# Kernel tuning notes

Measured on AMD Instinct MI355X. Metric: run time of the kernel, lower is better.

Reference implementation:

```python
import jax, jax.numpy as jnp
import numpy as np

N_NODES = 170000
N_EDGES = 1200000
IN_FEATS = 128
N_HIDDEN = 256
N_CLASSES = 40
BN_EPS = 1e-5


def setup_inputs() -> dict:
    key = jax.random.key(0)
    ks = jax.random.split(key, 12)
    feat = jax.random.normal(ks[0], (N_NODES, IN_FEATS), dtype=jnp.float32)
    src = jax.random.randint(ks[1], (N_EDGES,), 0, N_NODES, dtype=jnp.int32)
    dst = jax.random.randint(ks[2], (N_EDGES,), 0, N_NODES, dtype=jnp.int32)
    # GraphConv weights (glorot-ish scale) and last-layer bias
    W0 = jax.random.normal(ks[3], (IN_FEATS, N_HIDDEN), dtype=jnp.float32) * (1.0 / np.sqrt(IN_FEATS))
    W1 = jax.random.normal(ks[4], (N_HIDDEN, N_HIDDEN), dtype=jnp.float32) * (1.0 / np.sqrt(N_HIDDEN))
    W2 = jax.random.normal(ks[5], (N_HIDDEN, N_CLASSES), dtype=jnp.float32) * (1.0 / np.sqrt(N_HIDDEN))
    b2 = jnp.zeros((N_CLASSES,), dtype=jnp.float32)
    # BatchNorm affine params for the two hidden layers
    g0 = jnp.ones((N_HIDDEN,), dtype=jnp.float32)
    beta0 = jnp.zeros((N_HIDDEN,), dtype=jnp.float32)
    g1 = jnp.ones((N_HIDDEN,), dtype=jnp.float32)
    beta1 = jnp.zeros((N_HIDDEN,), dtype=jnp.float32)
    return {"feat": feat, "src": src, "dst": dst, "W0": W0, "W1": W1, "W2": W2,
            "b2": b2, "g0": g0, "beta0": beta0, "g1": g1, "beta1": beta1}


def _batchnorm(h, gamma, beta):
    mean = jnp.mean(h, axis=0)
    var = jnp.mean((h - mean) ** 2, axis=0)  # biased var, torch training-mode norm
    return (h - mean) * jax.lax.rsqrt(var + BN_EPS) * gamma + beta


def reference(feat, src, dst, W0, W1, W2, b2, g0, beta0, g1, beta1):
    n = feat.shape[0]
    ones_e = jnp.ones(src.shape, dtype=feat.dtype)
    deg_out = jnp.clip(jax.ops.segment_sum(ones_e, src, num_segments=n), 1.0)
    deg_in = jnp.clip(jax.ops.segment_sum(ones_e, dst, num_segments=n), 1.0)
    norm_src = deg_out ** -0.5  # [N]
    norm_dst = deg_in ** -0.5   # [N]

    def conv(h, W, bias=None):
        # GraphConv 'both': D_out^{-1/2} message, sum-aggregate, D_in^{-1/2}
        h = h @ W                              # project first (out <= in)
        msg = h[src] * norm_src[src][:, None]  # [E, out]
        agg = jax.ops.segment_sum(msg, dst, num_segments=n) * norm_dst[:, None]
        if bias is not None:
            agg = agg + bias
        return agg

    # dropout layers are identity in this deterministic (eval-style) reference
    h = conv(feat, W0)
    h = jax.nn.relu(_batchnorm(h, g0, beta0))
    h = conv(h, W1)
    h = jax.nn.relu(_batchnorm(h, g1, beta1))
    h = conv(h, W2, b2)
    return h
```

## Files before the change

### kernel.cpp

```cpp
#include <hip/hip_runtime.h>

#define NN 170000
#define NE 1200000
#define F_IN 128
#define F_HID 256
#define F_OUT 40
#define BN_EPS 1e-5f
#define SCAN_B ((NN + 255) / 256)
#define GB32 ((NN + 31) / 32)
#define GB128 ((NN + 127) / 128)
#define STAT_ROWS GB32
#define STAT_CHUNK 32
#define STAT_NCH ((STAT_ROWS + STAT_CHUNK - 1) / STAT_CHUNK)

typedef __attribute__((ext_vector_type(8))) short short8;
typedef __attribute__((ext_vector_type(4))) float f32x4;
typedef __attribute__((ext_vector_type(4))) unsigned short us4;
typedef __attribute__((ext_vector_type(4))) unsigned int u32x4;

__device__ __forceinline__ float b2f(unsigned short u) {
    union { unsigned x; float f; } c; c.x = ((unsigned)u) << 16; return c.f;
}
__device__ __forceinline__ unsigned short f2b(float f) {
    union { float f; unsigned x; } c; c.f = f;
    unsigned r = (c.x + 0x7FFFu + ((c.x >> 16) & 1u)) >> 16;
    return (unsigned short)r;
}
__device__ __forceinline__ unsigned bn2(unsigned u, float a0, float b0, float a1, float b1) {
    float lo = b2f((unsigned short)(u & 0xffffu));
    float hi = b2f((unsigned short)(u >> 16));
    lo = fmaxf(lo * a0 + b0, 0.0f);
    hi = fmaxf(hi * a1 + b1, 0.0f);
    return (unsigned)f2b(lo) | ((unsigned)f2b(hi) << 16);
}

__device__ __forceinline__ void agg_sum(const u32x4& v, float (&aa)[8]) {
    aa[0] += b2f((unsigned short)(v.x & 0xffffu)); aa[1] += b2f((unsigned short)(v.x >> 16));
    aa[2] += b2f((unsigned short)(v.y & 0xffffu)); aa[3] += b2f((unsigned short)(v.y >> 16));
    aa[4] += b2f((unsigned short)(v.z & 0xffffu)); aa[5] += b2f((unsigned short)(v.z >> 16));
    aa[6] += b2f((unsigned short)(v.w & 0xffffu)); aa[7] += b2f((unsigned short)(v.w >> 16));
}
__device__ __forceinline__ void agg_fuse(const u32x4& v, float ns,
        const f32x4& ca0, const f32x4& ca1, const f32x4& cb0, const f32x4& cb1, float (&aa)[8]) {
    aa[0] += fmaxf(fmaf(b2f((unsigned short)(v.x & 0xffffu)), ca0.x, cb0.x), 0.f) * ns;
    aa[1] += fmaxf(fmaf(b2f((unsigned short)(v.x >> 16)),     ca0.y, cb0.y), 0.f) * ns;
    aa[2] += fmaxf(fmaf(b2f((unsigned short)(v.y & 0xffffu)), ca0.z, cb0.z), 0.f) * ns;
    aa[3] += fmaxf(fmaf(b2f((unsigned short)(v.y >> 16)),     ca0.w, cb0.w), 0.f) * ns;
    aa[4] += fmaxf(fmaf(b2f((unsigned short)(v.z & 0xffffu)), ca1.x, cb1.x), 0.f) * ns;
    aa[5] += fmaxf(fmaf(b2f((unsigned short)(v.z >> 16)),     ca1.y, cb1.y), 0.f) * ns;
    aa[6] += fmaxf(fmaf(b2f((unsigned short)(v.w & 0xffffu)), ca1.z, cb1.z), 0.f) * ns;
    aa[7] += fmaxf(fmaf(b2f((unsigned short)(v.w >> 16)),     ca1.w, cb1.w), 0.f) * ns;
}

__global__ void count_kernel(const int* __restrict__ src, const int* __restrict__ dst,
                             int* __restrict__ cnt_src, int* __restrict__ cnt_dst, int E) {
    int e = blockIdx.x * blockDim.x + threadIdx.x;
    if (e < E) {
        atomicAdd(&cnt_src[src[e]], 1);
        atomicAdd(&cnt_dst[dst[e]], 1);
    }
}

__global__ void norm_kernel(const int* __restrict__ cnt_src, const int* __restrict__ cnt_dst,
                            float* __restrict__ norm_src, float* __restrict__ norm_dst, int N) {
    int i = blockIdx.x * blockDim.x + threadIdx.x;
    if (i < N) {
        norm_src[i] = rsqrtf((float)max(cnt_src[i], 1));
        norm_dst[i] = rsqrtf((float)max(cnt_dst[i], 1));
    }
}

__global__ void scan_block_kernel(const int* __restrict__ cnt, int* __restrict__ local,
                                  int* __restrict__ partials, int N) {
    __shared__ int s[256];
    int t = threadIdx.x;
    int idx = blockIdx.x * 256 + t;
    int v = (idx < N) ? cnt[idx] : 0;
    s[t] = v;
    __syncthreads();
    #pragma unroll
    for (int off = 1; off < 256; off <<= 1) {
        int x = (t >= off) ? s[t - off] : 0;
        __syncthreads();
        s[t] += x;
        __syncthreads();
    }
    if (idx < N) local[idx] = s[t] - v;
    if (t == 255) partials[blockIdx.x] = s[t];
}

__global__ void scan_partials_kernel(int* __restrict__ partials, int B) {
    __shared__ int s[1024];
    int t = threadIdx.x;
    int v = (t < B) ? partials[t] : 0;
    s[t] = v;
    __syncthreads();
    #pragma unroll
    for (int off = 1; off < 1024; off <<= 1) {
        int x = (t >= off) ? s[t - off] : 0;
        __syncthreads();
        s[t] += x;
        __syncthreads();
    }
    if (t < B) partials[t] = s[t] - v;
}

__global__ void scan_add_kernel(const int* __restrict__ local, const int* __restrict__ partials,
                                int* __restrict__ row_ptr, int N) {
    int idx = blockIdx.x * blockDim.x + threadIdx.x;
    if (idx < N) row_ptr[idx] = local[idx] + partials[idx >> 8];
    if (idx == 0) row_ptr[N] = NE;
}

__global__ void fill_kernel(const int* __restrict__ src, const int* __restrict__ dst,
                            const int* __restrict__ row_ptr, int* __restrict__ fill,
                            int* __restrict__ csr_src, int E) {
    int e = blockIdx.x * blockDim.x + threadIdx.x;
    if (e < E) {
        int d = dst[e];
        int pos = row_ptr[d] + atomicAdd(&fill[d], 1);
        csr_src[pos] = src[e];
    }
}

__global__ void cast_feat_kernel(const float* __restrict__ feat, const float* __restrict__ norm_src,
                                 unsigned short* __restrict__ featb) {
    unsigned idx = blockIdx.x * blockDim.x + threadIdx.x;
    if (idx >= (unsigned)NN * (F_IN / 4)) return;
    float ns = norm_src[idx / (F_IN / 4)];
    f32x4 v = __builtin_nontemporal_load((const f32x4*)(feat + (size_t)idx * 4));
    us4 o; o.x = f2b(v.x * ns); o.y = f2b(v.y * ns); o.z = f2b(v.z * ns); o.w = f2b(v.w * ns);
    *(us4*)(featb + (size_t)idx * 4) = o;
}

template<int K, int M, int MP>
__global__ void wt_kernel(const float* __restrict__ W, unsigned short* __restrict__ Wt) {
    int idx = blockIdx.x * blockDim.x + threadIdx.x;
    if (idx >= MP * K) return;
    int m = idx / K, k = idx % K;
    float v = (m < M) ? W[(size_t)k * M + m] : 0.0f;
    Wt[idx] = f2b(v);
}

__global__ void stat_reduce_kernel(const float* __restrict__ part, float* __restrict__ red) {
    int c = threadIdx.x;
    int ch = blockIdx.x;
    int r0 = ch * STAT_CHUNK;
    int r1 = min(r0 + STAT_CHUNK, STAT_ROWS);
    float s = 0.f;
    for (int r = r0; r < r1; r++) s += part[(size_t)r * 512 + c];
    red[ch * 512 + c] = s;
}

__global__ void bn_finalize2_kernel(const float* __restrict__ red,
                                    const float* __restrict__ gamma, const float* __restrict__ beta,
                                    float* __restrict__ a, float* __restrict__ b) {
    int c = threadIdx.x;
    float sum = 0.f, sumsq = 0.f;
    for (int ch = 0; ch < STAT_NCH; ch++) {
        sum   += red[ch * 512 + c];
        sumsq += red[ch * 512 + 256 + c];
    }
    float invN = 1.0f / (float)NN;
    float mean = sum * invN;
    float var = sumsq * invN - mean * mean;
    float inv = rsqrtf(var + BN_EPS);
    float ac = inv * gamma[c];
    a[c] = ac;
    b[c] = beta[c] - mean * ac;
}

template<int F, int WM_T, int WN_T, int WAVES_N, bool FUSE>
__global__ __launch_bounds__(256) void fused_gather_gemm(
        const unsigned short* __restrict__ h,
        const int* __restrict__ row_ptr, const int* __restrict__ csr_src,
        const float* __restrict__ bna, const float* __restrict__ bnb,
        const unsigned short* __restrict__ Wt,
        const float* __restrict__ norm_src, const float* __restrict__ norm_dst,
        void* __restrict__ C, float* __restrict__ opart, int N) {
    constexpr int WAVES_M = 4 / WAVES_N;
    constexpr int BM = WM_T * 16 * WAVES_M;
    constexpr int LPN = F / 8;
    constexpr int NPW = 64 / LPN;
    constexpr int NPB = BM / 4;
    __shared__ unsigned short As[BM * F];

    const int lane = threadIdx.x & 63;
    const int wave = threadIdx.x >> 6;
    const int r0 = blockIdx.x * BM;

    {
        const int sub = lane / LPN;
        const int cl = lane % LPN;
        f32x4 ca0 = {0,0,0,0}, ca1 = {0,0,0,0}, cb0 = {0,0,0,0}, cb1 = {0,0,0,0};
        if (FUSE) {
            ca0 = *(const f32x4*)(bna + cl * 8);
            ca1 = *(const f32x4*)(bna + cl * 8 + 4);
            cb0 = *(const f32x4*)(bnb + cl * 8);
            cb1 = *(const f32x4*)(bnb + cl * 8 + 4);
        }
        #pragma unroll
        for (int g = 0; g < NPB / NPW; g++) {
            int nl = wave * NPB + g * NPW + sub;
            int node = r0 + nl;
            float aa[8] = {0.f, 0.f, 0.f, 0.f, 0.f, 0.f, 0.f, 0.f};
            int beg = 0, end = 0;
            if (node < N) { beg = row_ptr[node]; end = row_ptr[node + 1]; }
            int e = beg;
            for (; e + 2 <= end; e += 2) {
                int s0 = csr_src[e], s1 = csr_src[e + 1];
                u32x4 v0 = *(const u32x4*)(h + (size_t)s0 * F + cl * 8);
                u32x4 v1 = *(const u32x4*)(h + (size_t)s1 * F + cl * 8);
                if (FUSE) {
                    float n0 = norm_src[s0], n1 = norm_src[s1];
                    agg_fuse(v0, n0, ca0, ca1, cb0, cb1, aa);
                    agg_fuse(v1, n1, ca0, ca1, cb0, cb1, aa);
                } else {
                    agg_sum(v0, aa); agg_sum(v1, aa);
                }
            }
            if (e < end) {
                int s0 = csr_src[e];
                u32x4 v0 = *(const u32x4*)(h + (size_t)s0 * F + cl * 8);
                if (FUSE) agg_fuse(v0, norm_src[s0], ca0, ca1, cb0, cb1, aa);
                else      agg_sum(v0, aa);
            }
            u32x4 d;
            d.x = (unsigned)f2b(aa[0]) | ((unsigned)f2b(aa[1]) << 16);
            d.y = (unsigned)f2b(aa[2]) | ((unsigned)f2b(aa[3]) << 16);
            d.z = (unsigned)f2b(aa[4]) | ((unsigned)f2b(aa[5]) << 16);
            d.w = (unsigned)f2b(aa[6]) | ((unsigned)f2b(aa[7]) << 16);
            unsigned off = ((unsigned)(nl * (F * 2) + cl * 16)) ^ (((unsigned)nl & 7u) << 4);
            *(u32x4*)((char*)As + off) = d;
        }
    }
    __syncthreads();

    const int quad = lane >> 4, l15 = lane & 15;
    const int wr = wave / WAVES_N, wc = wave % WAVES_N;
    const int wmb = wr * WM_T * 16;
    const int wnb = wc * WN_T * 16;

    const unsigned short* bptr[WN_T];
    #pragma unroll
    for (int j = 0; j < WN_T; j++)
        bptr[j] = Wt + (size_t)(wnb + j * 16 + l15) * F + quad * 8;

    f32x4 acc[WM_T][WN_T] = {};
    #pragma unroll
    for (int kk = 0; kk < F; kk += 32) {
        short8 af[WM_T], bf[WN_T];
        #pragma unroll
        for (int i = 0; i < WM_T; i++) {
            int row = wmb + i * 16 + l15;
            unsigned off = ((unsigned)(row * (F * 2) + (kk + quad * 8) * 2)) ^ (((unsigned)row & 7u) << 4);
            af[i] = *(const short8*)((const char*)As + off);
        }
        #pragma unroll
        for (int j = 0; j < WN_T; j++)
            bf[j] = *(const short8*)(bptr[j] + kk);
        #pragma unroll
        for (int i = 0; i < WM_T; i++)
            #pragma unroll
            for (int j = 0; j < WN_T; j++)
                acc[i][j] = __builtin_amdgcn_mfma_f32_16x16x32_bf16(af[i], bf[j], acc[i][j], 0, 0, 0);
    }

    float s[WN_T] = {}, ss[WN_T] = {};
    #pragma unroll
    for (int i = 0; i < WM_T; i++) {
        #pragma unroll
        for (int r = 0; r < 4; r++) {
            int row = r0 + wmb + i * 16 + quad * 4 + r;
            if (row >= N) continue;
            float nd = norm_dst[row];
            #pragma unroll
            for (int j = 0; j < WN_T; j++) {
                float v = acc[i][j][r] * nd;
                int col = wnb + j * 16 + l15;
                s[j] += v; ss[j] += v * v;
                ((unsigned short*)C)[(size_t)row * F_HID + col] = f2b(v);
            }
        }
    }
    #pragma unroll
    for (int j = 0; j < WN_T; j++) {
        float t = s[j], t2 = ss[j];
        t  += __shfl_xor(t, 16);  t  += __shfl_xor(t, 32);
        t2 += __shfl_xor(t2, 16); t2 += __shfl_xor(t2, 32);
        if (quad == 0) {
            int col = wnb + j * 16 + l15;
            size_t prow = (size_t)(blockIdx.x * WAVES_M + wr) * 512;
            opart[prow + col] = t;
            opart[prow + 256 + col] = t2;
        }
    }
}

__global__ __launch_bounds__(256, 3) void gemm2_kernel(const unsigned short* __restrict__ A,
                                                       const unsigned short* __restrict__ Wt,
                                                       const float* __restrict__ norm_src,
                                                       const float* __restrict__ bna,
                                                       const float* __restrict__ bnb,
                                                       float* __restrict__ C, int N) {
    constexpr int K = 256, WM_T = 2, WN_T = 4;
    const int lane = threadIdx.x & 63;
    const int wave = threadIdx.x >> 6;
    const int quad = lane >> 4, l15 = lane & 15;
    const int r0 = blockIdx.x * 128;
    const int wmb = wave * WM_T * 16;

    const unsigned short* aptr[WM_T];
    #pragma unroll
    for (int i = 0; i < WM_T; i++) {
        int gr = r0 + wmb + i * 16 + l15;
        if (gr > N - 1) gr = N - 1;
        aptr[i] = A + (size_t)gr * K + quad * 8;
    }
    const unsigned short* bptr[WN_T];
    #pragma unroll
    for (int j = 0; j < WN_T; j++)
        bptr[j] = Wt + (size_t)(j * 16 + l15) * K + quad * 8;

    f32x4 acc[WM_T][WN_T] = {};
    #pragma unroll
    for (int kk = 0; kk < K; kk += 32) {
        int kb = kk + quad * 8;
        const f32x4 a0 = *(const f32x4*)(bna + kb);
        const f32x4 a1 = *(const f32x4*)(bna + kb + 4);
        const f32x4 s0 = *(const f32x4*)(bnb + kb);
        const f32x4 s1 = *(const f32x4*)(bnb + kb + 4);
        short8 af[WM_T], bf[WN_T];
        #pragma unroll
        for (int i = 0; i < WM_T; i++) {
            u32x4 u = *(const u32x4*)(aptr[i] + kk);
            u.x = bn2(u.x, a0.x, s0.x, a0.y, s0.y);
            u.y = bn2(u.y, a0.z, s0.z, a0.w, s0.w);
            u.z = bn2(u.z, a1.x, s1.x, a1.y, s1.y);
            u.w = bn2(u.w, a1.z, s1.z, a1.w, s1.w);
            af[i] = *(short8*)&u;
        }
        #pragma unroll
        for (int j = 0; j < WN_T; j++)
            bf[j] = *(const short8*)(bptr[j] + kk);
        #pragma unroll
        for (int i = 0; i < WM_T; i++)
            #pragma unroll
            for (int j = 0; j < WN_T; j++)
                acc[i][j] = __builtin_amdgcn_mfma_f32_16x16x32_bf16(af[i], bf[j], acc[i][j], 0, 0, 0);
    }

    #pragma unroll
    for (int i = 0; i < WM_T; i++) {
        #pragma unroll
        for (int r = 0; r < 4; r++) {
            int row = r0 + wmb + i * 16 + quad * 4 + r;
            if (row >= N) continue;
            float ns = norm_src[row];
            #pragma unroll
            for (int j = 0; j < WN_T; j++) {
                int col = j * 16 + l15;
                if (col < F_OUT)
                    C[(size_t)row * F_OUT + col] = acc[i][j][r] * ns;
            }
        }
    }
}

__global__ void gather_final_kernel(const float* __restrict__ h, const int* __restrict__ row_ptr,
                                    const int* __restrict__ csr_src,
                                    const float* __restrict__ norm_dst, const float* __restrict__ bias,
                                    float* __restrict__ out, int N) {
    constexpr int TPN = F_OUT / 4;
    unsigned idx = blockIdx.x * blockDim.x + threadIdx.x;
    if (idx >= (unsigned)N * TPN) return;
    unsigned node = idx / TPN;
    unsigned g = idx % TPN;
    int beg = row_ptr[node], end = row_ptr[node + 1];
    float ax0 = 0.f, ay0 = 0.f, az0 = 0.f, aw0 = 0.f;
    float ax1 = 0.f, ay1 = 0.f, az1 = 0.f, aw1 = 0.f;
    int e = beg;
    for (; e + 2 <= end; e += 2) {
        int s0 = csr_src[e], s1 = csr_src[e + 1];
        const f32x4 v0 = *(const f32x4*)(h + (size_t)s0 * F_OUT + g * 4);
        const f32x4 v1 = *(const f32x4*)(h + (size_t)s1 * F_OUT + g * 4);
        ax0 += v0.x; ay0 += v0.y; az0 += v0.z; aw0 += v0.w;
        ax1 += v1.x; ay1 += v1.y; az1 += v1.z; aw1 += v1.w;
    }
    if (e < end) {
        int s0 = csr_src[e];
        const f32x4 v0 = *(const f32x4*)(h + (size_t)s0 * F_OUT + g * 4);
        ax0 += v0.x; ay0 += v0.y; az0 += v0.z; aw0 += v0.w;
    }
    float nd = norm_dst[node];
    const f32x4 b = *(const f32x4*)(bias + g * 4);
    f32x4 r;
    r.x = (ax0 + ax1) * nd + b.x; r.y = (ay0 + ay1) * nd + b.y;
    r.z = (az0 + az1) * nd + b.z; r.w = (aw0 + aw1) * nd + b.w;
    __builtin_nontemporal_store(r, (f32x4*)(out + (size_t)node * F_OUT + g * 4));
}

extern "C" void kernel_launch(void* const* d_in, const int* in_sizes, int n_in,
                              void* d_out, int out_size, void* d_ws, size_t ws_size,
                              hipStream_t stream) {
    const float* feat  = (const float*)d_in[0];
    const int*   src   = (const int*)d_in[1];
    const int*   dst   = (const int*)d_in[2];
    const float* W0    = (const float*)d_in[3];
    const float* W1    = (const float*)d_in[4];
    const float* W2    = (const float*)d_in[5];
    const float* b2    = (const float*)d_in[6];
    const float* g0    = (const float*)d_in[7];
    const float* beta0 = (const float*)d_in[8];
    const float* g1    = (const float*)d_in[9];
    const float* beta1 = (const float*)d_in[10];
    float* out = (float*)d_out;

    const int N = NN, E = NE;

    char* ws = (char*)d_ws;
    auto alloc_b = [&](size_t bytes) {
        void* p = (void*)ws;
        ws += ((bytes + 255) / 256) * 256;
        return p;
    };
    float* norm_src = (float*)alloc_b((size_t)N * 4);
    float* norm_dst = (float*)alloc_b((size_t)N * 4);
    int*   row_ptr  = (int*)alloc_b((size_t)(N + 1) * 4);
    int*   csr_src  = (int*)alloc_b((size_t)E * 4);
    float* bnpart   = (float*)alloc_b((size_t)STAT_ROWS * 512 * 4);
    float* bnred    = (float*)alloc_b((size_t)STAT_NCH * 512 * 4);
    float* bn_a0    = (float*)alloc_b(256 * 4);
    float* bn_b0    = (float*)alloc_b(256 * 4);
    float* bn_a1    = (float*)alloc_b(256 * 4);
    float* bn_b1    = (float*)alloc_b(256 * 4);
    unsigned short* Wt0 = (unsigned short*)alloc_b((size_t)256 * 128 * 2);
    unsigned short* Wt1 = (unsigned short*)alloc_b((size_t)256 * 256 * 2);
    unsigned short* Wt2 = (unsigned short*)alloc_b((size_t)64 * 256 * 2);
    void* B1 = alloc_b((size_t)N * 512);
    void* B2 = alloc_b((size_t)N * 512);
    unsigned short* featb = (unsigned short*)alloc_b((size_t)N * F_IN * 2);

    unsigned short* B1b = (unsigned short*)B1;
    unsigned short* B2b = (unsigned short*)B2;
    float*          B1f = (float*)B1;

    int* cnt_src  = (int*)B1;
    int* cnt_dst  = cnt_src + N;
    int* fill     = cnt_dst + N;
    int* local    = fill + N;
    int* partials = local + N;

    hipMemsetAsync(cnt_src, 0, ((size_t)4 * N + 1024) * 4, stream);
    count_kernel<<<(E + 255) / 256, 256, 0, stream>>>(src, dst, cnt_src, cnt_dst, E);
    norm_kernel<<<(N + 255) / 256, 256, 0, stream>>>(cnt_src, cnt_dst, norm_src, norm_dst, N);
    scan_block_kernel<<<SCAN_B, 256, 0, stream>>>(cnt_dst, local, partials, N);
    scan_partials_kernel<<<1, 1024, 0, stream>>>(partials, SCAN_B);
    scan_add_kernel<<<(N + 255) / 256, 256, 0, stream>>>(local, partials, row_ptr, N);
    fill_kernel<<<(E + 255) / 256, 256, 0, stream>>>(src, dst, row_ptr, fill, csr_src, E);
    wt_kernel<128, 256, 256><<<(256 * 128 + 255) / 256, 256, 0, stream>>>(W0, Wt0);
    wt_kernel<256, 256, 256><<<(256 * 256 + 255) / 256, 256, 0, stream>>>(W1, Wt1);
    wt_kernel<256, 40, 64><<<(64 * 256 + 255) / 256, 256, 0, stream>>>(W2, Wt2);
    cast_feat_kernel<<<((unsigned)N * (F_IN / 4) + 255) / 256, 256, 0, stream>>>(feat, norm_src, featb);

    fused_gather_gemm<128, 2, 4, 4, false><<<GB32, 256, 0, stream>>>(
        featb, row_ptr, csr_src, nullptr, nullptr, Wt0, nullptr, norm_dst, B1, bnpart, N);
    stat_reduce_kernel<<<STAT_NCH, 512, 0, stream>>>(bnpart, bnred);
    bn_finalize2_kernel<<<1, 256, 0, stream>>>(bnred, g0, beta0, bn_a0, bn_b0);

    fused_gather_gemm<256, 2, 4, 4, true><<<GB32, 256, 0, stream>>>(
        B1b, row_ptr, csr_src, bn_a0, bn_b0, Wt1, norm_src, norm_dst, B2, bnpart, N);
    stat_reduce_kernel<<<STAT_NCH, 512, 0, stream>>>(bnpart, bnred);
    bn_finalize2_kernel<<<1, 256, 0, stream>>>(bnred, g1, beta1, bn_a1, bn_b1);

    gemm2_kernel<<<GB128, 256, 0, stream>>>(B2b, Wt2, norm_src, bn_a1, bn_b1, B1f, N);
    {
        unsigned total = (unsigned)N * (F_OUT / 4);
        gather_final_kernel<<<(total + 255) / 256, 256, 0, stream>>>(
            B1f, row_ptr, csr_src, norm_dst, b2, out, N);
    }
}
```

Measured before the change: 763.6 us.

## Make each wave own 16 rows independently in fused gather-GEMM, drop block barrier

Each wave now gathers its own 16 destination rows into a private LDS slice and computes all 256 output columns for them, looping over 16 column tiles. This removes the block-wide __syncthreads between gather and GEMM, so waves with short neighbour lists can move on without waiting for the slowest wave. Blocks now cover 64 rows instead of 32, with matching changes to the BN partial-stat row count. The cost is less reuse of weight fragments: every wave streams the whole W matrix from global or L2 memory per 16 rows, and each MFMA chain now works on a single accumulator, which gives less instruction-level parallelism.

```diff
diff --git a/kernel.cpp b/kernel.cpp
--- a/kernel.cpp
+++ b/kernel.cpp
@@ -7,9 +7,9 @@
 #define F_OUT 40
 #define BN_EPS 1e-5f
 #define SCAN_B ((NN + 255) / 256)
-#define GB32 ((NN + 31) / 32)
+#define GB64 ((NN + 63) / 64)
 #define GB128 ((NN + 127) / 128)
-#define STAT_ROWS GB32
+#define STAT_ROWS (4 * GB64)
 #define STAT_CHUNK 32
 #define STAT_NCH ((STAT_ROWS + STAT_CHUNK - 1) / STAT_CHUNK)
 
@@ -170,7 +170,7 @@
     b[c] = beta[c] - mean * ac;
 }
 
-template<int F, int WM_T, int WN_T, int WAVES_N, bool FUSE>
+template<int F, bool FUSE>
 __global__ __launch_bounds__(256) void fused_gather_gemm(
         const unsigned short* __restrict__ h,
         const int* __restrict__ row_ptr, const int* __restrict__ csr_src,
@@ -178,16 +178,15 @@
         const unsigned short* __restrict__ Wt,
         const float* __restrict__ norm_src, const float* __restrict__ norm_dst,
         void* __restrict__ C, float* __restrict__ opart, int N) {
-    constexpr int WAVES_M = 4 / WAVES_N;
-    constexpr int BM = WM_T * 16 * WAVES_M;
     constexpr int LPN = F / 8;
     constexpr int NPW = 64 / LPN;
-    constexpr int NPB = BM / 4;
-    __shared__ unsigned short As[BM * F];
+    constexpr int GROUPS = 16 / NPW;
+    __shared__ unsigned short As[64 * F];
 
     const int lane = threadIdx.x & 63;
     const int wave = threadIdx.x >> 6;
-    const int r0 = blockIdx.x * BM;
+    const int r0 = blockIdx.x * 64 + wave * 16;
+    char* Aw = (char*)(As + wave * 16 * F);
 
     {
         const int sub = lane / LPN;
@@ -200,8 +199,8 @@
             cb1 = *(const f32x4*)(bnb + cl * 8 + 4);
         }
         #pragma unroll
-        for (int g = 0; g < NPB / NPW; g++) {
-            int nl = wave * NPB + g * NPW + sub;
+        for (int g = 0; g < GROUPS; g++) {
+            int nl = g * NPW + sub;
             int node = r0 + nl;
             float aa[8] = {0.f, 0.f, 0.f, 0.f, 0.f, 0.f, 0.f, 0.f};
             int beg = 0, end = 0;
@@ -231,68 +230,43 @@
             d.z = (unsigned)f2b(aa[4]) | ((unsigned)f2b(aa[5]) << 16);
             d.w = (unsigned)f2b(aa[6]) | ((unsigned)f2b(aa[7]) << 16);
             unsigned off = ((unsigned)(nl * (F * 2) + cl * 16)) ^ (((unsigned)nl & 7u) << 4);
-            *(u32x4*)((char*)As + off) = d;
-        }
-    }
-    __syncthreads();
+            *(u32x4*)(Aw + off) = d;
+        }
+    }
 
     const int quad = lane >> 4, l15 = lane & 15;
-    const int wr = wave / WAVES_N, wc = wave % WAVES_N;
-    const int wmb = wr * WM_T * 16;
-    const int wnb = wc * WN_T * 16;
-
-    const unsigned short* bptr[WN_T];
-    #pragma unroll
-    for (int j = 0; j < WN_T; j++)
-        bptr[j] = Wt + (size_t)(wnb + j * 16 + l15) * F + quad * 8;
-
-    f32x4 acc[WM_T][WN_T] = {};
-    #pragma unroll
-    for (int kk = 0; kk < F; kk += 32) {
-        short8 af[WM_T], bf[WN_T];
-        #pragma unroll
-        for (int i = 0; i < WM_T; i++) {
-            int row = wmb + i * 16 + l15;
-            unsigned off = ((unsigned)(row * (F * 2) + (kk + quad * 8) * 2)) ^ (((unsigned)row & 7u) << 4);
-            af[i] = *(const short8*)((const char*)As + off);
-        }
-        #pragma unroll
-        for (int j = 0; j < WN_T; j++)
-            bf[j] = *(const short8*)(bptr[j] + kk);
-        #pragma unroll
-        for (int i = 0; i < WM_T; i++)
-            #pragma unroll
-            for (int j = 0; j < WN_T; j++)
-                acc[i][j] = __builtin_amdgcn_mfma_f32_16x16x32_bf16(af[i], bf[j], acc[i][j], 0, 0, 0);
-    }
-
-    float s[WN_T] = {}, ss[WN_T] = {};
-    #pragma unroll
-    for (int i = 0; i < WM_T; i++) {
+    const size_t prow = (size_t)(blockIdx.x * 4 + wave) * 512;
+    float nd[4];
+    #pragma unroll
+    for (int r = 0; r < 4; r++) {
+        int row = r0 + quad * 4 + r;
+        nd[r] = (row < N) ? norm_dst[row] : 0.0f;
+    }
+    #pragma unroll 2
+    for (int jt = 0; jt < 16; jt++) {
+        const unsigned short* bptr = Wt + (size_t)(jt * 16 + l15) * F + quad * 8;
+        f32x4 acc = {0.f, 0.f, 0.f, 0.f};
+        #pragma unroll
+        for (int kk = 0; kk < F; kk += 32) {
+            unsigned off = ((unsigned)(l15 * (F * 2) + (kk + quad * 8) * 2)) ^ (((unsigned)l15 & 7u) << 4);
+            short8 af = *(const short8*)(Aw + off);
+            short8 bf = *(const short8*)(bptr + kk);
+            acc = __builtin_amdgcn_mfma_f32_16x16x32_bf16(af, bf, acc, 0, 0, 0);
+        }
+        float s_ = 0.f, ss_ = 0.f;
         #pragma unroll
         for (int r = 0; r < 4; r++) {
-            int row = r0 + wmb + i * 16 + quad * 4 + r;
-            if (row >= N) continue;
-            float nd = norm_dst[row];
-            #pragma unroll
-            for (int j = 0; j < WN_T; j++) {
-                float v = acc[i][j][r] * nd;
-                int col = wnb + j * 16 + l15;
-                s[j] += v; ss[j] += v * v;
-                ((unsigned short*)C)[(size_t)row * F_HID + col] = f2b(v);
-            }
-        }
-    }
-    #pragma unroll
-    for (int j = 0; j < WN_T; j++) {
-        float t = s[j], t2 = ss[j];
-        t  += __shfl_xor(t, 16);  t  += __shfl_xor(t, 32);
-        t2 += __shfl_xor(t2, 16); t2 += __shfl_xor(t2, 32);
+            int row = r0 + quad * 4 + r;
+            float v = acc[r] * nd[r];
+            s_ += v; ss_ += v * v;
+            if (row < N)
+                ((unsigned short*)C)[(size_t)row * F_HID + jt * 16 + l15] = f2b(v);
+        }
+        s_  += __shfl_xor(s_, 16);  s_  += __shfl_xor(s_, 32);
+        ss_ += __shfl_xor(ss_, 16); ss_ += __shfl_xor(ss_, 32);
         if (quad == 0) {
-            int col = wnb + j * 16 + l15;
-            size_t prow = (size_t)(blockIdx.x * WAVES_M + wr) * 512;
-            opart[prow + col] = t;
-            opart[prow + 256 + col] = t2;
+            opart[prow + jt * 16 + l15] = s_;
+            opart[prow + 256 + jt * 16 + l15] = ss_;
         }
     }
 }
@@ -463,12 +437,12 @@
     wt_kernel<256, 40, 64><<<(64 * 256 + 255) / 256, 256, 0, stream>>>(W2, Wt2);
     cast_feat_kernel<<<((unsigned)N * (F_IN / 4) + 255) / 256, 256, 0, stream>>>(feat, norm_src, featb);
 
-    fused_gather_gemm<128, 2, 4, 4, false><<<GB32, 256, 0, stream>>>(
+    fused_gather_gemm<128, false><<<GB64, 256, 0, stream>>>(
         featb, row_ptr, csr_src, nullptr, nullptr, Wt0, nullptr, norm_dst, B1, bnpart, N);
     stat_reduce_kernel<<<STAT_NCH, 512, 0, stream>>>(bnpart, bnred);
     bn_finalize2_kernel<<<1, 256, 0, stream>>>(bnred, g0, beta0, bn_a0, bn_b0);
 
-    fused_gather_gemm<256, 2, 4, 4, true><<<GB32, 256, 0, stream>>>(
+    fused_gather_gemm<256, true><<<GB64, 256, 0, stream>>>(
         B1b, row_ptr, csr_src, bn_a0, bn_b0, Wt1, norm_src, norm_dst, B2, bnpart, N);
     stat_reduce_kernel<<<STAT_NCH, 512, 0, stream>>>(bnpart, bnred);
     bn_finalize2_kernel<<<1, 256, 0, stream>>>(bnred, g1, beta1, bn_a1, bn_b1);
```

New measurement: 868.0 us. +13.7%, slower.
